# Kernel tuning notes

Measured on AMD Instinct MI355X. Metric: run time of the kernel, lower is better.

## Reference

```python
import jax, jax.numpy as jnp
import numpy as np

D_MODEL = 1024
NUM_HEADS = 16
HEAD_DIM = D_MODEL // NUM_HEADS

def setup_inputs() -> dict:
    key = jax.random.key(0)
    ks = jax.random.split(key, 5)
    B, T = 4, 2048
    x = jax.random.normal(ks[0], (B, T, D_MODEL), dtype=jnp.float32)
    s = 1.0 / np.sqrt(D_MODEL)
    W_qkv = jax.random.normal(ks[1], (D_MODEL, 3 * D_MODEL), dtype=jnp.float32) * s
    b_qkv = jnp.zeros((3 * D_MODEL,), dtype=jnp.float32)
    W_out = jax.random.normal(ks[2], (D_MODEL, D_MODEL), dtype=jnp.float32) * s
    b_out = jnp.zeros((D_MODEL,), dtype=jnp.float32)
    return {"x": x, "W_qkv": W_qkv, "b_qkv": b_qkv, "W_out": W_out, "b_out": b_out}

def reference(x, W_qkv, b_qkv, W_out, b_out):
    B, T, C = x.shape
    H, Dh = NUM_HEADS, HEAD_DIM
    qkv = x @ W_qkv + b_qkv                      # [B,T,3C]
    qkv = qkv.reshape(B, T, 3, H, Dh)
    q = jnp.transpose(qkv[:, :, 0], (0, 2, 1, 3))  # [B,H,T,Dh]
    k = jnp.transpose(qkv[:, :, 1], (0, 2, 1, 3))
    v = jnp.transpose(qkv[:, :, 2], (0, 2, 1, 3))
    scores = jnp.einsum('bhqd,bhkd->bhqk', q, k) / jnp.sqrt(jnp.asarray(Dh, x.dtype))
    weights = jax.nn.softmax(scores, axis=-1)
    out = jnp.einsum('bhqk,bhkd->bhqd', weights, v)  # [B,H,T,Dh]
    out = jnp.transpose(out, (0, 2, 1, 3)).reshape(B, T, C)
    return out @ W_out + b_out
```

## Files before the change

### kernel.cpp

```cpp
#include <hip/hip_runtime.h>
#include <stdint.h>

typedef __bf16 bf16x8 __attribute__((ext_vector_type(8)));
typedef float f32x4 __attribute__((ext_vector_type(4)));
typedef float f32x16 __attribute__((ext_vector_type(16)));

static constexpr int BB = 4, TT = 2048, CC = 1024, HH = 16, DH = 64;
static constexpr int MM = BB * TT;
static constexpr int N1 = 3 * CC;
static constexpr int KK = CC;

__device__ __forceinline__ unsigned short f2bf(float f) {
  uint32_t u = __builtin_bit_cast(uint32_t, f);
  u += 0x7FFFu + ((u >> 16) & 1u);
  return (unsigned short)(u >> 16);
}

__device__ __forceinline__ void async16(const void* g, void* l) {
  __builtin_amdgcn_global_load_lds((const __attribute__((address_space(1))) void*)g,
                                   (__attribute__((address_space(3))) void*)l, 16, 0, 0);
}

__global__ __launch_bounds__(256) void k_cvt(const float* __restrict__ src,
                                             unsigned short* __restrict__ dst) {
  int i = blockIdx.x * 256 + threadIdx.x;
  const float4* s = (const float4*)src + (size_t)i * 2;
  float4 a = s[0], b = s[1];
  union { unsigned short h[8]; uint4 v; } o;
  o.h[0] = f2bf(a.x); o.h[1] = f2bf(a.y); o.h[2] = f2bf(a.z); o.h[3] = f2bf(a.w);
  o.h[4] = f2bf(b.x); o.h[5] = f2bf(b.y); o.h[6] = f2bf(b.z); o.h[7] = f2bf(b.w);
  ((uint4*)dst)[i] = o.v;
}

__global__ __launch_bounds__(256) void k_tcvt(const float* __restrict__ src,
                                              unsigned short* __restrict__ dst,
                                              int R, int C) {
  __shared__ float tile[32][33];
  int tx = threadIdx.x & 31, ty = threadIdx.x >> 5;
  int c0 = blockIdx.x * 32, r0 = blockIdx.y * 32;
#pragma unroll
  for (int i = 0; i < 4; ++i)
    tile[ty + i * 8][tx] = src[(size_t)(r0 + ty + i * 8) * C + c0 + tx];
  __syncthreads();
#pragma unroll
  for (int i = 0; i < 4; ++i)
    dst[(size_t)(c0 + ty + i * 8) * R + r0 + tx] = f2bf(tile[tx][ty + i * 8]);
}


#define LDA(Ab, mf, ksl) \
  (*(const bf16x8*)&(Ab)[wm * 8192 + ((mf) * 16 + l15) * 64 + \
                         ((((ksl) * 4 + l16) ^ (l15 & 7)) * 8)])
#define LDB(Bb, nf, ksl) \
  (*(const bf16x8*)&(Bb)[(wn >> 1) * 8192 + ((wn & 1) * 64 + (nf) * 16 + l15) * 64 + \
                         ((((ksl) * 4 + l16) ^ (l15 & 7)) * 8)])

struct AF4 { bf16x8 a00, a01, a10, a11; };

template <int Q, bool LOADB>
__device__ __forceinline__ AF4 phase_pre(const unsigned short* Ab, const unsigned short* Bb,
                                         int wm, int wn, int l15, int l16, bf16x8* bfr) {
  AF4 f;
  f.a00 = LDA(Ab, Q * 2, 0);     f.a01 = LDA(Ab, Q * 2, 1);
  f.a10 = LDA(Ab, Q * 2 + 1, 0); f.a11 = LDA(Ab, Q * 2 + 1, 1);
  if (LOADB) {
#pragma unroll
    for (int nf = 0; nf < 4; ++nf) {
      bfr[nf] = LDB(Bb, nf, 0);
      bfr[4 + nf] = LDB(Bb, nf, 1);
    }
  }
  return f;
}

template <int Q>
__device__ __forceinline__ void phase_mfma(const AF4& f, const bf16x8* bfr, f32x4 acc[8][4]) {
#pragma unroll
  for (int nf = 0; nf < 4; ++nf)
    acc[Q * 2][nf] = __builtin_amdgcn_mfma_f32_16x16x32_bf16(f.a00, bfr[nf], acc[Q * 2][nf], 0, 0, 0);
#pragma unroll
  for (int nf = 0; nf < 4; ++nf)
    acc[Q * 2][nf] = __builtin_amdgcn_mfma_f32_16x16x32_bf16(f.a01, bfr[4 + nf], acc[Q * 2][nf], 0, 0, 0);
#pragma unroll
  for (int nf = 0; nf < 4; ++nf)
    acc[Q * 2 + 1][nf] = __builtin_amdgcn_mfma_f32_16x16x32_bf16(f.a10, bfr[nf], acc[Q * 2 + 1][nf], 0, 0, 0);
#pragma unroll
  for (int nf = 0; nf < 4; ++nf)
    acc[Q * 2 + 1][nf] = __builtin_amdgcn_mfma_f32_16x16x32_bf16(f.a11, bfr[4 + nf], acc[Q * 2 + 1][nf], 0, 0, 0);
}

#define PHASE(Q, AB, BB_, LOADB, STAGES, WAITS)                       \
  { AF4 f_ = phase_pre<Q, LOADB>(AB, BB_, wm, wn, l15, l16, bfr);     \
    STAGES;                                                           \
    WAITS;                                                            \
    __builtin_amdgcn_s_barrier();                                     \
    asm volatile("s_waitcnt lgkmcnt(0)" ::: "memory");                \
    __builtin_amdgcn_sched_barrier(0);                                \
    __builtin_amdgcn_s_setprio(1);                                    \
    phase_mfma<Q>(f_, bfr, acc);                                      \
    __builtin_amdgcn_s_setprio(0);                                    \
    __builtin_amdgcn_s_barrier(); }

template <int MODE, int NBX>
__global__ __launch_bounds__(512, 2) void k_gemm8(
    const unsigned short* __restrict__ A, const unsigned short* __restrict__ Bt,
    const float* __restrict__ bias, int M, int N, int K,
    unsigned short* __restrict__ qo, unsigned short* __restrict__ ko,
    unsigned short* __restrict__ vo, float* __restrict__ fo) {
  __shared__ __attribute__((aligned(16))) unsigned short lds[65536];
  unsigned short* As0 = lds;
  unsigned short* As1 = lds + 16384;
  unsigned short* Bs0 = lds + 32768;
  unsigned short* Bs1 = lds + 49152;

  const int tid = threadIdx.x;
  const int lane = tid & 63;
  const int w = tid >> 6, wm = w >> 2, wn = w & 3;
  const int l15 = lane & 15, l16 = lane >> 4;

  const int nwg = gridDim.x;
  const int q8 = nwg >> 3;
  const int swz = ((int)blockIdx.x & 7) * q8 + ((int)blockIdx.x >> 3);
  const int m0 = (swz / NBX) * 256, n0 = (swz % NBX) * 256;

  f32x4 acc[8][4] = {};

  const int srow = tid >> 3;
  const int sg = ((tid & 7) ^ (srow & 7)) * 8;
  const int dOff = srow * 64 + (tid & 7) * 8;
  const unsigned short* aBase = A + (size_t)(m0 + srow) * K + sg;
  const unsigned short* bBase = Bt + (size_t)(n0 + srow) * K + sg;

#define STAGE_A(dst, kt, h)                                                          \
  { async16(aBase + (size_t)((h) * 128) * K + (kt) * 64, (dst) + (h) * 8192 + dOff); \
    async16(aBase + (size_t)((h) * 128 + 64) * K + (kt) * 64,                        \
            (dst) + (h) * 8192 + 4096 + dOff); }
#define STAGE_B(dst, kt, h)                                                          \
  { async16(bBase + (size_t)((h) * 128) * K + (kt) * 64, (dst) + (h) * 8192 + dOff); \
    async16(bBase + (size_t)((h) * 128 + 64) * K + (kt) * 64,                        \
            (dst) + (h) * 8192 + 4096 + dOff); }

  STAGE_A(As0, 0, 0); STAGE_A(As0, 0, 1);
  STAGE_B(Bs0, 0, 0); STAGE_B(Bs0, 0, 1);
  STAGE_B(Bs1, 1, 0); STAGE_B(Bs1, 1, 1);
  asm volatile("s_waitcnt vmcnt(0)" ::: "memory");
  __builtin_amdgcn_s_barrier();

  const int NITER = K / 128;
#pragma unroll 1
  for (int i = 0; i < NITER; ++i) {
    const bool more = (i + 1 < NITER);
    const int t1 = 2 * i + 1, t2k = 2 * i + 2, t3 = 2 * i + 3;
    bf16x8 bfr[8];
    PHASE(0, As0, Bs0, true,  { STAGE_A(As1, t1, 0); }, ((void)0));
    PHASE(1, As0, Bs0, false, { STAGE_A(As1, t1, 1); }, ((void)0));
    PHASE(2, As0, Bs0, false, { if (more) STAGE_B(Bs0, t2k, 0); }, ((void)0));
    PHASE(3, As0, Bs0, false, { if (more) STAGE_B(Bs0, t2k, 1); },
          { if (more) { asm volatile("s_waitcnt vmcnt(4)" ::: "memory"); }
            else      { asm volatile("s_waitcnt vmcnt(0)" ::: "memory"); } });
    PHASE(0, As1, Bs1, true,  { if (more) STAGE_A(As0, t2k, 0); }, ((void)0));
    PHASE(1, As1, Bs1, false, { if (more) STAGE_A(As0, t2k, 1); }, ((void)0));
    PHASE(2, As1, Bs1, false, { if (more) STAGE_B(Bs1, t3, 0); }, ((void)0));
    PHASE(3, As1, Bs1, false, { if (more) STAGE_B(Bs1, t3, 1); },
          { asm volatile("s_waitcnt vmcnt(4)" ::: "memory"); });
  }

  if (MODE == 0) {
    const int sel = n0 >> 10;
    if (sel < 2) {
      const float qs = (sel == 0) ? 0.180336892f : 1.0f;
      float bj[4];
#pragma unroll
      for (int nf = 0; nf < 4; ++nf) bj[nf] = bias[n0 + wn * 64 + nf * 16 + l15];
#pragma unroll
      for (int mf = 0; mf < 8; ++mf)
#pragma unroll
        for (int nf = 0; nf < 4; ++nf)
#pragma unroll
          for (int r = 0; r < 4; ++r) {
            const int row = wm * 128 + mf * 16 + l16 * 4 + r;
            const int col = wn * 64 + nf * 16 + l15;
            lds[row * 256 + (((col >> 3) ^ (row & 31)) * 8) + (col & 7)] =
                f2bf((acc[mf][nf][r] + bj[nf]) * qs);
          }
      __syncthreads();
      const int row = tid >> 1, half = tid & 1;
      const int gm = m0 + row, bb2 = gm >> 11, t2 = gm & 2047;
      const int hb = ((n0 & 1023) >> 6) + half * 2;
      unsigned short* base = (sel == 0 ? qo : ko);
#pragma unroll
      for (int hh = 0; hh < 2; ++hh) {
        unsigned short* dst = base + ((size_t)(bb2 * HH + hb + hh) * TT + t2) * DH;
#pragma unroll
        for (int g = 0; g < 8; ++g) {
          const int cg = half * 16 + hh * 8 + g;
          bf16x8 v = *(const bf16x8*)&lds[row * 256 + ((cg ^ (row & 31)) * 8)];
          *(bf16x8*)&dst[g * 8] = v;
        }
      }
    } else {
#pragma unroll
      for (int mf = 0; mf < 8; ++mf)
#pragma unroll
        for (int nf = 0; nf < 4; ++nf) {
          const int gn = n0 + wn * 64 + nf * 16 + l15;
          const float bj = bias[gn];
          const int h = (gn & 1023) >> 6, d = gn & 63;
          const int gm0 = m0 + wm * 128 + mf * 16 + l16 * 4;
          const int bb2 = gm0 >> 11, t0 = gm0 & 2047;
          union { unsigned short s[4]; uint2 u; } pk;
#pragma unroll
          for (int r = 0; r < 4; ++r) pk.s[r] = f2bf(acc[mf][nf][r] + bj);
          *(uint2*)&vo[((size_t)(bb2 * HH + h) * DH + d) * TT + t0] = pk.u;
        }
    }
  } else {
#pragma unroll
    for (int mf = 0; mf < 8; ++mf)
#pragma unroll
      for (int nf = 0; nf < 4; ++nf) {
        const int gn = n0 + wn * 64 + nf * 16 + l15;
        const float bj = bias[gn];
#pragma unroll
        for (int r = 0; r < 4; ++r) {
          const int gm = m0 + wm * 128 + mf * 16 + l16 * 4 + r;
          fo[(size_t)gm * N + gn] = acc[mf][nf][r] + bj;
        }
      }
  }
#undef STAGE_A
#undef STAGE_B
}

__global__ __launch_bounds__(256, 2) void k_attn(
    const unsigned short* __restrict__ Q,
    const unsigned short* __restrict__ Kx,
    const unsigned short* __restrict__ Vt,
    unsigned short* __restrict__ At,
    float neg16) {
  __shared__ __attribute__((aligned(16))) unsigned short Ks[2][64 * 64];
  __shared__ __attribute__((aligned(16))) unsigned short Vs[2][64 * 64];
  const int tid = threadIdx.x, lane = tid & 63, w = tid >> 6;
  const int l31 = lane & 31, hi5 = lane >> 5;
  const int id = blockIdx.x;
  const int bh = (id & 7) + ((id >> 7) << 3);
  const int qb = (id >> 3) & 15;
  const int q0 = qb * 128 + w * 32;
  const unsigned short* Qp = Q + (size_t)bh * TT * DH;
  const unsigned short* Kp = Kx + (size_t)bh * TT * DH;
  const unsigned short* Vp = Vt + (size_t)bh * DH * TT;

  bf16x8 qf[4];
#pragma unroll
  for (int j = 0; j < 4; ++j)
    qf[j] = *(const bf16x8*)&Qp[(size_t)(q0 + l31) * DH + j * 16 + hi5 * 8];

  f32x16 cinit;
#pragma unroll
  for (int r = 0; r < 16; ++r) cinit[r] = neg16;

  const int srow = tid >> 3;
  const int sg = ((tid & 7) ^ (srow & 7)) * 8;

  float l8[8];
#pragma unroll
  for (int r = 0; r < 8; ++r) l8[r] = 0.f;
  f32x16 oacc[2] = {};

#pragma unroll
  for (int i = 0; i < 2; ++i) {
    async16(Kp + (size_t)(i * 32 + srow) * DH + sg, &Ks[0][i * 2048 + tid * 8]);
    async16(Vp + (size_t)(i * 32 + srow) * TT + sg, &Vs[0][i * 2048 + tid * 8]);
  }
  __syncthreads();

#pragma unroll 2
  for (int kt = 0; kt < TT / 64; ++kt) {
    const int cur = kt & 1;
    if (kt + 1 < TT / 64) {
      const int kv1 = (kt + 1) * 64;
#pragma unroll
      for (int i = 0; i < 2; ++i) {
        async16(Kp + (size_t)(kv1 + i * 32 + srow) * DH + sg,
                &Ks[cur ^ 1][i * 2048 + tid * 8]);
        async16(Vp + (size_t)(i * 32 + srow) * TT + kv1 + sg,
                &Vs[cur ^ 1][i * 2048 + tid * 8]);
      }
    }

    f32x16 sacc[2];
    __builtin_amdgcn_s_setprio(1);
#pragma unroll
    for (int t = 0; t < 2; ++t) {
      bf16x8 kf = *(const bf16x8*)&Ks[cur][(t * 32 + l31) * 64 +
                      ((hi5 ^ (l31 & 7)) * 8)];
      sacc[t] = __builtin_amdgcn_mfma_f32_32x32x16_bf16(kf, qf[0], cinit, 0, 0, 0);
    }
#pragma unroll
    for (int ks16 = 1; ks16 < 4; ++ks16) {
#pragma unroll
      for (int t = 0; t < 2; ++t) {
        bf16x8 kf = *(const bf16x8*)&Ks[cur][(t * 32 + l31) * 64 +
                        (((ks16 * 2 + hi5) ^ (l31 & 7)) * 8)];
        sacc[t] = __builtin_amdgcn_mfma_f32_32x32x16_bf16(kf, qf[ks16], sacc[t], 0, 0, 0);
      }
    }
    __builtin_amdgcn_s_setprio(0);
    asm volatile("" : "+v"(sacc[0]), "+v"(sacc[1]));

#pragma unroll
    for (int t = 0; t < 2; ++t)
#pragma unroll
      for (int r = 0; r < 16; ++r)
        sacc[t][r] = __builtin_amdgcn_exp2f(sacc[t][r]);
#pragma unroll
    for (int r = 0; r < 8; ++r)
      l8[r] += (sacc[0][r] + sacc[0][r + 8]) + (sacc[1][r] + sacc[1][r + 8]);

    uint32_t wpk[16];
#pragma unroll
    for (int t = 0; t < 2; ++t) {
      union { __bf16 h[16]; uint32_t u[8]; } pk;
#pragma unroll
      for (int r = 0; r < 16; ++r) pk.h[r] = (__bf16)sacc[t][r];
#pragma unroll
      for (int j = 0; j < 8; ++j) wpk[t * 8 + j] = pk.u[j];
    }
    uint32_t xw[8];
#pragma unroll
    for (int t = 0; t < 2; ++t) {
      xw[t * 4 + 0] = __shfl_xor(hi5 ? wpk[t * 8 + 0] : wpk[t * 8 + 2], 32);
      xw[t * 4 + 1] = __shfl_xor(hi5 ? wpk[t * 8 + 1] : wpk[t * 8 + 3], 32);
      xw[t * 4 + 2] = __shfl_xor(hi5 ? wpk[t * 8 + 4] : wpk[t * 8 + 6], 32);
      xw[t * 4 + 3] = __shfl_xor(hi5 ? wpk[t * 8 + 5] : wpk[t * 8 + 7], 32);
    }

    __builtin_amdgcn_s_setprio(1);
#pragma unroll
    for (int ks = 0; ks < 4; ++ks) {
      const int t = ks >> 1, b = (ks & 1) * 4, o = t * 8, xb = t * 4 + (ks & 1) * 2;
      union { uint32_t u[4]; bf16x8 v; } pu;
      pu.u[0] = hi5 ? xw[xb] : wpk[o + b];
      pu.u[1] = hi5 ? xw[xb + 1] : wpk[o + b + 1];
      pu.u[2] = hi5 ? wpk[o + b + 2] : xw[xb];
      pu.u[3] = hi5 ? wpk[o + b + 3] : xw[xb + 1];
#pragma unroll
      for (int dt = 0; dt < 2; ++dt) {
        bf16x8 vf = *(const bf16x8*)&Vs[cur][(dt * 32 + l31) * 64 +
                        (((ks * 2 + hi5) ^ (l31 & 7)) * 8)];
        oacc[dt] = __builtin_amdgcn_mfma_f32_32x32x16_bf16(vf, pu.v, oacc[dt], 0, 0, 0);
      }
    }
    __builtin_amdgcn_s_setprio(0);
    __syncthreads();
  }

  float l = ((l8[0] + l8[4]) + (l8[1] + l8[5])) +
            ((l8[2] + l8[6]) + (l8[3] + l8[7]));
  l += __shfl_xor(l, 32);

  const float il = 1.0f / l;
  unsigned short* bw = &Ks[0][0] + w * 2048;
#pragma unroll
  for (int dt = 0; dt < 2; ++dt)
#pragma unroll
    for (int j = 0; j < 8; ++j) {
      const int dl = (j & 1) * 2 + (j >> 1) * 8 + hi5 * 4;
      const int d = dt * 32 + dl;
      const uint32_t pk = (uint32_t)f2bf(oacc[dt][2 * j] * il) |
                          ((uint32_t)f2bf(oacc[dt][2 * j + 1] * il) << 16);
      const int g = d >> 3, gi = (d >> 1) & 3;
      *(uint32_t*)&bw[l31 * 64 + ((g ^ (l31 & 7)) * 8) + gi * 2] = pk;
    }
  __syncthreads();
  const int bb = bh >> 4, hd = bh & 15;
#pragma unroll
  for (int i = 0; i < 4; ++i) {
    const int row = i * 8 + (lane >> 3);
    const int g = lane & 7;
    bf16x8 vv = *(const bf16x8*)&bw[row * 64 + ((g ^ (row & 7)) * 8)];
    *(bf16x8*)&At[((size_t)bb * TT + q0 + row) * CC + hd * DH + g * 8] = vv;
  }
}

extern "C" void kernel_launch(void* const* d_in, const int* in_sizes, int n_in,
                              void* d_out, int out_size, void* d_ws, size_t ws_size,
                              hipStream_t stream) {
  const float* x = (const float*)d_in[0];
  const float* Wqkv = (const float*)d_in[1];
  const float* bqkv = (const float*)d_in[2];
  const float* Wout = (const float*)d_in[3];
  const float* bout = (const float*)d_in[4];
  float* out = (float*)d_out;

  char* ws = (char*)d_ws;
  unsigned short* Xb  = (unsigned short*)(ws);
  unsigned short* WqT = (unsigned short*)(ws + (16ull << 20));
  unsigned short* WoT = (unsigned short*)(ws + (22ull << 20));
  unsigned short* Qb  = (unsigned short*)(ws + (24ull << 20));
  unsigned short* Kb  = (unsigned short*)(ws + (40ull << 20));
  unsigned short* Vt  = (unsigned short*)(ws + (56ull << 20));
  unsigned short* At  = (unsigned short*)(ws + (72ull << 20));

  k_cvt<<<dim3((MM * KK) / (256 * 8)), 256, 0, stream>>>(x, Xb);
  k_tcvt<<<dim3(N1 / 32, KK / 32), 256, 0, stream>>>(Wqkv, WqT, KK, N1);
  k_tcvt<<<dim3(CC / 32, KK / 32), 256, 0, stream>>>(Wout, WoT, KK, CC);
  k_gemm8<0, 12><<<dim3((N1 / 256) * (MM / 256)), 512, 0, stream>>>(
      Xb, WqT, bqkv, MM, N1, KK, Qb, Kb, Vt, nullptr);
  k_attn<<<dim3(BB * HH * (TT / 128)), 256, 0, stream>>>(Qb, Kb, Vt, At, -16.0f);
  k_gemm8<1, 4><<<dim3((CC / 256) * (MM / 256)), 512, 0, stream>>>(
      At, WoT, bout, MM, CC, KK, nullptr, nullptr, nullptr, out);
}
```

Baseline: 212.7 us.

## Use smaller-tile GEMM for output projection and relax attention loop barriers

The output projection moves from the 256x256-tile pipelined GEMM to a new 128x128-tile kernel with 256 threads. That launches 512 workgroups instead of 128, so more compute units are filled. The new kernel has no double buffering and no LDS swizzle, so load latency and LDS bank conflicts may be exposed. The attention loop now always prefetches the next K/V tile and replaces `__syncthreads` with explicit `vmcnt`/`lgkmcnt` waits plus `s_barrier`, so loads overlap compute. The trade-off is that the last iteration reads one tile beyond the current head's K/V data.

```diff
diff --git a/kernel.cpp b/kernel.cpp
--- a/kernel.cpp
+++ b/kernel.cpp
@@ -46,7 +46,6 @@
   for (int i = 0; i < 4; ++i)
     dst[(size_t)(c0 + ty + i * 8) * R + r0 + tx] = f2bf(tile[tx][ty + i * 8]);
 }
-
 
 #define LDA(Ab, mf, ksl) \
   (*(const bf16x8*)&(Ab)[wm * 8192 + ((mf) * 16 + l15) * 64 + \
@@ -101,12 +100,12 @@
     __builtin_amdgcn_s_setprio(0);                                    \
     __builtin_amdgcn_s_barrier(); }
 
-template <int MODE, int NBX>
+template <int NBX>
 __global__ __launch_bounds__(512, 2) void k_gemm8(
     const unsigned short* __restrict__ A, const unsigned short* __restrict__ Bt,
     const float* __restrict__ bias, int M, int N, int K,
     unsigned short* __restrict__ qo, unsigned short* __restrict__ ko,
-    unsigned short* __restrict__ vo, float* __restrict__ fo) {
+    unsigned short* __restrict__ vo) {
   __shared__ __attribute__((aligned(16))) unsigned short lds[65536];
   unsigned short* As0 = lds;
   unsigned short* As1 = lds + 16384;
@@ -165,54 +164,37 @@
           { asm volatile("s_waitcnt vmcnt(4)" ::: "memory"); });
   }
 
-  if (MODE == 0) {
-    const int sel = n0 >> 10;
-    if (sel < 2) {
-      const float qs = (sel == 0) ? 0.180336892f : 1.0f;
-      float bj[4];
-#pragma unroll
-      for (int nf = 0; nf < 4; ++nf) bj[nf] = bias[n0 + wn * 64 + nf * 16 + l15];
-#pragma unroll
-      for (int mf = 0; mf < 8; ++mf)
-#pragma unroll
-        for (int nf = 0; nf < 4; ++nf)
-#pragma unroll
-          for (int r = 0; r < 4; ++r) {
-            const int row = wm * 128 + mf * 16 + l16 * 4 + r;
-            const int col = wn * 64 + nf * 16 + l15;
-            lds[row * 256 + (((col >> 3) ^ (row & 31)) * 8) + (col & 7)] =
-                f2bf((acc[mf][nf][r] + bj[nf]) * qs);
-          }
-      __syncthreads();
-      const int row = tid >> 1, half = tid & 1;
-      const int gm = m0 + row, bb2 = gm >> 11, t2 = gm & 2047;
-      const int hb = ((n0 & 1023) >> 6) + half * 2;
-      unsigned short* base = (sel == 0 ? qo : ko);
-#pragma unroll
-      for (int hh = 0; hh < 2; ++hh) {
-        unsigned short* dst = base + ((size_t)(bb2 * HH + hb + hh) * TT + t2) * DH;
-#pragma unroll
-        for (int g = 0; g < 8; ++g) {
-          const int cg = half * 16 + hh * 8 + g;
-          bf16x8 v = *(const bf16x8*)&lds[row * 256 + ((cg ^ (row & 31)) * 8)];
-          *(bf16x8*)&dst[g * 8] = v;
+  const int sel = n0 >> 10;
+  if (sel < 2) {
+    const float qs = (sel == 0) ? 0.180336892f : 1.0f;
+    float bj[4];
+#pragma unroll
+    for (int nf = 0; nf < 4; ++nf) bj[nf] = bias[n0 + wn * 64 + nf * 16 + l15];
+#pragma unroll
+    for (int mf = 0; mf < 8; ++mf)
+#pragma unroll
+      for (int nf = 0; nf < 4; ++nf)
+#pragma unroll
+        for (int r = 0; r < 4; ++r) {
+          const int row = wm * 128 + mf * 16 + l16 * 4 + r;
+          const int col = wn * 64 + nf * 16 + l15;
+          lds[row * 256 + (((col >> 3) ^ (row & 31)) * 8) + (col & 7)] =
+              f2bf((acc[mf][nf][r] + bj[nf]) * qs);
         }
+    __syncthreads();
+    const int row = tid >> 1, half = tid & 1;
+    const int gm = m0 + row, bb2 = gm >> 11, t2 = gm & 2047;
+    const int hb = ((n0 & 1023) >> 6) + half * 2;
+    unsigned short* base = (sel == 0 ? qo : ko);
+#pragma unroll
+    for (int hh = 0; hh < 2; ++hh) {
+      unsigned short* dst = base + ((size_t)(bb2 * HH + hb + hh) * TT + t2) * DH;
+#pragma unroll
+      for (int g = 0; g < 8; ++g) {
+        const int cg = half * 16 + hh * 8 + g;
+        bf16x8 v = *(const bf16x8*)&lds[row * 256 + ((cg ^ (row & 31)) * 8)];
+        *(bf16x8*)&dst[g * 8] = v;
       }
-    } else {
-#pragma unroll
-      for (int mf = 0; mf < 8; ++mf)
-#pragma unroll
-        for (int nf = 0; nf < 4; ++nf) {
-          const int gn = n0 + wn * 64 + nf * 16 + l15;
-          const float bj = bias[gn];
-          const int h = (gn & 1023) >> 6, d = gn & 63;
-          const int gm0 = m0 + wm * 128 + mf * 16 + l16 * 4;
-          const int bb2 = gm0 >> 11, t0 = gm0 & 2047;
-          union { unsigned short s[4]; uint2 u; } pk;
-#pragma unroll
-          for (int r = 0; r < 4; ++r) pk.s[r] = f2bf(acc[mf][nf][r] + bj);
-          *(uint2*)&vo[((size_t)(bb2 * HH + h) * DH + d) * TT + t0] = pk.u;
-        }
     }
   } else {
 #pragma unroll
@@ -221,15 +203,76 @@
       for (int nf = 0; nf < 4; ++nf) {
         const int gn = n0 + wn * 64 + nf * 16 + l15;
         const float bj = bias[gn];
-#pragma unroll
-        for (int r = 0; r < 4; ++r) {
-          const int gm = m0 + wm * 128 + mf * 16 + l16 * 4 + r;
-          fo[(size_t)gm * N + gn] = acc[mf][nf][r] + bj;
-        }
+        const int h = (gn & 1023) >> 6, d = gn & 63;
+        const int gm0 = m0 + wm * 128 + mf * 16 + l16 * 4;
+        const int bb2 = gm0 >> 11, t0 = gm0 & 2047;
+        union { unsigned short s[4]; uint2 u; } pk;
+#pragma unroll
+        for (int r = 0; r < 4; ++r) pk.s[r] = f2bf(acc[mf][nf][r] + bj);
+        *(uint2*)&vo[((size_t)(bb2 * HH + h) * DH + d) * TT + t0] = pk.u;
       }
   }
 #undef STAGE_A
 #undef STAGE_B
+}
+
+__global__ __launch_bounds__(256) void k_gemmB(
+    const unsigned short* __restrict__ A, const unsigned short* __restrict__ Bt,
+    const float* __restrict__ bias, int M, int N, int K,
+    float* __restrict__ fo) {
+  __shared__ __attribute__((aligned(16))) unsigned short As[128 * 64];
+  __shared__ __attribute__((aligned(16))) unsigned short Bs[128 * 64];
+  const int tid = threadIdx.x;
+  const int lane = tid & 63;
+  const int w = tid >> 6, wr = w >> 1, wc = w & 1;
+  const int l15 = lane & 15, l16 = lane >> 4;
+  const int m0 = blockIdx.y * 128, n0 = blockIdx.x * 128;
+
+  f32x4 acc[4][4] = {};
+
+  const unsigned short* aSrc = A + (size_t)(m0 + (tid >> 3)) * K + (tid & 7) * 8;
+  const unsigned short* bSrc = Bt + (size_t)(n0 + (tid >> 3)) * K + (tid & 7) * 8;
+  unsigned short* aDst = &As[tid * 8];
+  unsigned short* bDst = &Bs[tid * 8];
+
+#pragma unroll 1
+  for (int k0 = 0; k0 < K; k0 += 64) {
+#pragma unroll
+    for (int i = 0; i < 4; ++i) {
+      async16(aSrc + (size_t)i * 32 * K + k0, aDst + i * 2048);
+      async16(bSrc + (size_t)i * 32 * K + k0, bDst + i * 2048);
+    }
+    __syncthreads();
+#pragma unroll
+    for (int ks = 0; ks < 2; ++ks) {
+      bf16x8 af[4], bfr[4];
+#pragma unroll
+      for (int i = 0; i < 4; ++i)
+        af[i] = *(const bf16x8*)&As[(wr * 64 + i * 16 + l15) * 64 + ks * 32 + l16 * 8];
+#pragma unroll
+      for (int j = 0; j < 4; ++j)
+        bfr[j] = *(const bf16x8*)&Bs[(wc * 64 + j * 16 + l15) * 64 + ks * 32 + l16 * 8];
+#pragma unroll
+      for (int i = 0; i < 4; ++i)
+#pragma unroll
+        for (int j = 0; j < 4; ++j)
+          acc[i][j] = __builtin_amdgcn_mfma_f32_16x16x32_bf16(af[i], bfr[j], acc[i][j], 0, 0, 0);
+    }
+    __syncthreads();
+  }
+
+#pragma unroll
+  for (int i = 0; i < 4; ++i)
+#pragma unroll
+    for (int j = 0; j < 4; ++j) {
+      const int gn = n0 + wc * 64 + j * 16 + l15;
+      const float bj = bias[gn];
+#pragma unroll
+      for (int r = 0; r < 4; ++r) {
+        const int gm = m0 + wr * 64 + i * 16 + l16 * 4 + r;
+        fo[(size_t)gm * N + gn] = acc[i][j][r] + bj;
+      }
+    }
 }
 
 __global__ __launch_bounds__(256, 2) void k_attn(
@@ -272,21 +315,21 @@
     async16(Kp + (size_t)(i * 32 + srow) * DH + sg, &Ks[0][i * 2048 + tid * 8]);
     async16(Vp + (size_t)(i * 32 + srow) * TT + sg, &Vs[0][i * 2048 + tid * 8]);
   }
-  __syncthreads();
 
 #pragma unroll 2
   for (int kt = 0; kt < TT / 64; ++kt) {
     const int cur = kt & 1;
-    if (kt + 1 < TT / 64) {
-      const int kv1 = (kt + 1) * 64;
-#pragma unroll
-      for (int i = 0; i < 2; ++i) {
-        async16(Kp + (size_t)(kv1 + i * 32 + srow) * DH + sg,
-                &Ks[cur ^ 1][i * 2048 + tid * 8]);
-        async16(Vp + (size_t)(i * 32 + srow) * TT + kv1 + sg,
-                &Vs[cur ^ 1][i * 2048 + tid * 8]);
-      }
-    }
+    const int kv1 = (kt + 1) * 64;
+#pragma unroll
+    for (int i = 0; i < 2; ++i) {
+      async16(Kp + (size_t)(kv1 + i * 32 + srow) * DH + sg,
+              &Ks[cur ^ 1][i * 2048 + tid * 8]);
+      async16(Vp + (size_t)(i * 32 + srow) * TT + kv1 + sg,
+              &Vs[cur ^ 1][i * 2048 + tid * 8]);
+    }
+    asm volatile("s_waitcnt vmcnt(4)" ::: "memory");
+    __builtin_amdgcn_sched_barrier(0);
+    __builtin_amdgcn_s_barrier();
 
     f32x16 sacc[2];
     __builtin_amdgcn_s_setprio(1);
@@ -352,8 +395,13 @@
       }
     }
     __builtin_amdgcn_s_setprio(0);
-    __syncthreads();
-  }
+    asm volatile("s_waitcnt lgkmcnt(0)" ::: "memory");
+    __builtin_amdgcn_sched_barrier(0);
+    __builtin_amdgcn_s_barrier();
+  }
+
+  asm volatile("s_waitcnt vmcnt(0)" ::: "memory");
+  __builtin_amdgcn_s_barrier();
 
   float l = ((l8[0] + l8[4]) + (l8[1] + l8[5])) +
             ((l8[2] + l8[6]) + (l8[3] + l8[7]));
@@ -405,9 +453,9 @@
   k_cvt<<<dim3((MM * KK) / (256 * 8)), 256, 0, stream>>>(x, Xb);
   k_tcvt<<<dim3(N1 / 32, KK / 32), 256, 0, stream>>>(Wqkv, WqT, KK, N1);
   k_tcvt<<<dim3(CC / 32, KK / 32), 256, 0, stream>>>(Wout, WoT, KK, CC);
-  k_gemm8<0, 12><<<dim3((N1 / 256) * (MM / 256)), 512, 0, stream>>>(
-      Xb, WqT, bqkv, MM, N1, KK, Qb, Kb, Vt, nullptr);
+  k_gemm8<12><<<dim3((N1 / 256) * (MM / 256)), 512, 0, stream>>>(
+      Xb, WqT, bqkv, MM, N1, KK, Qb, Kb, Vt);
   k_attn<<<dim3(BB * HH * (TT / 128)), 256, 0, stream>>>(Qb, Kb, Vt, At, -16.0f);
-  k_gemm8<1, 4><<<dim3((CC / 256) * (MM / 256)), 512, 0, stream>>>(
-      At, WoT, bout, MM, CC, KK, nullptr, nullptr, nullptr, out);
-}
+  k_gemmB<<<dim3(CC / 128, MM / 128), 256, 0, stream>>>(
+      At, WoT, bout, MM, CC, KK, out);
+}
```

After: 216.9 us. Within noise of the previous version (+2.0%).

## Shrink GEMM tiles to 256x128 with reworked phase schedule and epilogue

Applied to the files above, without the earlier changes.

Both projection GEMMs move from 256x256 to 256x128 output tiles. Per-wave accumulators are halved, B staging now covers 128 rows, and each k-step runs two phases instead of four, with new waitcnt values and a new LDS epilogue layout. The aim is to double the workgroup count (768 and 256 tiles) for better CU fill on the MI355X and to cut LDS and register use. The cost is lower arithmetic intensity per tile, more A-tile reloads, and fewer MFMAs per barrier to hide the sync overhead.

```diff
diff --git a/kernel.cpp b/kernel.cpp
--- a/kernel.cpp
+++ b/kernel.cpp
@@ -48,82 +48,81 @@
 }
 
 
-#define LDA(Ab, mf, ksl) \
-  (*(const bf16x8*)&(Ab)[wm * 8192 + ((mf) * 16 + l15) * 64 + \
+#define LDA4(Ab, mf, ksl) \
+  (*(const bf16x8*)&(Ab)[(wm * 128 + (mf) * 16 + l15) * 64 + \
                          ((((ksl) * 4 + l16) ^ (l15 & 7)) * 8)])
-#define LDB(Bb, nf, ksl) \
-  (*(const bf16x8*)&(Bb)[(wn >> 1) * 8192 + ((wn & 1) * 64 + (nf) * 16 + l15) * 64 + \
+#define LDB4(Bb, nf, ksl) \
+  (*(const bf16x8*)&(Bb)[(wn * 32 + (nf) * 16 + l15) * 64 + \
                          ((((ksl) * 4 + l16) ^ (l15 & 7)) * 8)])
 
-struct AF4 { bf16x8 a00, a01, a10, a11; };
-
-template <int Q, bool LOADB>
-__device__ __forceinline__ AF4 phase_pre(const unsigned short* Ab, const unsigned short* Bb,
-                                         int wm, int wn, int l15, int l16, bf16x8* bfr) {
-  AF4 f;
-  f.a00 = LDA(Ab, Q * 2, 0);     f.a01 = LDA(Ab, Q * 2, 1);
-  f.a10 = LDA(Ab, Q * 2 + 1, 0); f.a11 = LDA(Ab, Q * 2 + 1, 1);
+struct AF8 { bf16x8 a[8]; };
+
+template <int P, bool LOADB>
+__device__ __forceinline__ AF8 phase_pre4(const unsigned short* Ab, const unsigned short* Bb,
+                                          int wm, int wn, int l15, int l16, bf16x8* bfr) {
+  AF8 f;
+#pragma unroll
+  for (int mf = 0; mf < 4; ++mf) {
+    f.a[mf * 2] = LDA4(Ab, P * 4 + mf, 0);
+    f.a[mf * 2 + 1] = LDA4(Ab, P * 4 + mf, 1);
+  }
   if (LOADB) {
 #pragma unroll
-    for (int nf = 0; nf < 4; ++nf) {
-      bfr[nf] = LDB(Bb, nf, 0);
-      bfr[4 + nf] = LDB(Bb, nf, 1);
+    for (int nf = 0; nf < 2; ++nf) {
+      bfr[nf * 2] = LDB4(Bb, nf, 0);
+      bfr[nf * 2 + 1] = LDB4(Bb, nf, 1);
     }
   }
   return f;
 }
 
-template <int Q>
-__device__ __forceinline__ void phase_mfma(const AF4& f, const bf16x8* bfr, f32x4 acc[8][4]) {
-#pragma unroll
-  for (int nf = 0; nf < 4; ++nf)
-    acc[Q * 2][nf] = __builtin_amdgcn_mfma_f32_16x16x32_bf16(f.a00, bfr[nf], acc[Q * 2][nf], 0, 0, 0);
-#pragma unroll
-  for (int nf = 0; nf < 4; ++nf)
-    acc[Q * 2][nf] = __builtin_amdgcn_mfma_f32_16x16x32_bf16(f.a01, bfr[4 + nf], acc[Q * 2][nf], 0, 0, 0);
-#pragma unroll
-  for (int nf = 0; nf < 4; ++nf)
-    acc[Q * 2 + 1][nf] = __builtin_amdgcn_mfma_f32_16x16x32_bf16(f.a10, bfr[nf], acc[Q * 2 + 1][nf], 0, 0, 0);
-#pragma unroll
-  for (int nf = 0; nf < 4; ++nf)
-    acc[Q * 2 + 1][nf] = __builtin_amdgcn_mfma_f32_16x16x32_bf16(f.a11, bfr[4 + nf], acc[Q * 2 + 1][nf], 0, 0, 0);
-}
-
-#define PHASE(Q, AB, BB_, LOADB, STAGES, WAITS)                       \
-  { AF4 f_ = phase_pre<Q, LOADB>(AB, BB_, wm, wn, l15, l16, bfr);     \
+template <int P>
+__device__ __forceinline__ void phase_mfma4(const AF8& f, const bf16x8* bfr, f32x4 acc[8][2]) {
+#pragma unroll
+  for (int mf = 0; mf < 4; ++mf)
+#pragma unroll
+    for (int nf = 0; nf < 2; ++nf) {
+      acc[P * 4 + mf][nf] = __builtin_amdgcn_mfma_f32_16x16x32_bf16(
+          f.a[mf * 2], bfr[nf * 2], acc[P * 4 + mf][nf], 0, 0, 0);
+      acc[P * 4 + mf][nf] = __builtin_amdgcn_mfma_f32_16x16x32_bf16(
+          f.a[mf * 2 + 1], bfr[nf * 2 + 1], acc[P * 4 + mf][nf], 0, 0, 0);
+    }
+}
+
+#define PHASE4(P, AB, BB_, LOADB, STAGES, WAITS)                      \
+  { AF8 f_ = phase_pre4<P, LOADB>(AB, BB_, wm, wn, l15, l16, bfr);    \
     STAGES;                                                           \
     WAITS;                                                            \
     __builtin_amdgcn_s_barrier();                                     \
     asm volatile("s_waitcnt lgkmcnt(0)" ::: "memory");                \
     __builtin_amdgcn_sched_barrier(0);                                \
     __builtin_amdgcn_s_setprio(1);                                    \
-    phase_mfma<Q>(f_, bfr, acc);                                      \
+    phase_mfma4<P>(f_, bfr, acc);                                     \
     __builtin_amdgcn_s_setprio(0);                                    \
     __builtin_amdgcn_s_barrier(); }
 
 template <int MODE, int NBX>
-__global__ __launch_bounds__(512, 2) void k_gemm8(
+__global__ __launch_bounds__(512, 2) void k_gemm4(
     const unsigned short* __restrict__ A, const unsigned short* __restrict__ Bt,
     const float* __restrict__ bias, int M, int N, int K,
     unsigned short* __restrict__ qo, unsigned short* __restrict__ ko,
     unsigned short* __restrict__ vo, float* __restrict__ fo) {
-  __shared__ __attribute__((aligned(16))) unsigned short lds[65536];
+  __shared__ __attribute__((aligned(16))) unsigned short lds[49152];
   unsigned short* As0 = lds;
   unsigned short* As1 = lds + 16384;
   unsigned short* Bs0 = lds + 32768;
-  unsigned short* Bs1 = lds + 49152;
+  unsigned short* Bs1 = lds + 40960;
 
   const int tid = threadIdx.x;
   const int lane = tid & 63;
   const int w = tid >> 6, wm = w >> 2, wn = w & 3;
   const int l15 = lane & 15, l16 = lane >> 4;
 
-  const int nwg = gridDim.x;
-  const int q8 = nwg >> 3;
+  const int q8 = (int)gridDim.x >> 3;
   const int swz = ((int)blockIdx.x & 7) * q8 + ((int)blockIdx.x >> 3);
-  const int m0 = (swz / NBX) * 256, n0 = (swz % NBX) * 256;
-
-  f32x4 acc[8][4] = {};
+  const int m0 = (swz / NBX) * 256, n0 = (swz % NBX) * 128;
+
+  f32x4 acc[8][2] = {};
 
   const int srow = tid >> 3;
   const int sg = ((tid & 7) ^ (srow & 7)) * 8;
@@ -135,14 +134,13 @@
   { async16(aBase + (size_t)((h) * 128) * K + (kt) * 64, (dst) + (h) * 8192 + dOff); \
     async16(aBase + (size_t)((h) * 128 + 64) * K + (kt) * 64,                        \
             (dst) + (h) * 8192 + 4096 + dOff); }
-#define STAGE_B(dst, kt, h)                                                          \
-  { async16(bBase + (size_t)((h) * 128) * K + (kt) * 64, (dst) + (h) * 8192 + dOff); \
-    async16(bBase + (size_t)((h) * 128 + 64) * K + (kt) * 64,                        \
-            (dst) + (h) * 8192 + 4096 + dOff); }
+#define STAGE_B(dst, kt)                                                             \
+  { async16(bBase + (kt) * 64, (dst) + dOff);                                        \
+    async16(bBase + (size_t)64 * K + (kt) * 64, (dst) + 4096 + dOff); }
 
   STAGE_A(As0, 0, 0); STAGE_A(As0, 0, 1);
-  STAGE_B(Bs0, 0, 0); STAGE_B(Bs0, 0, 1);
-  STAGE_B(Bs1, 1, 0); STAGE_B(Bs1, 1, 1);
+  STAGE_B(Bs0, 0);
+  STAGE_B(Bs1, 1);
   asm volatile("s_waitcnt vmcnt(0)" ::: "memory");
   __builtin_amdgcn_s_barrier();
 
@@ -150,60 +148,57 @@
 #pragma unroll 1
   for (int i = 0; i < NITER; ++i) {
     const bool more = (i + 1 < NITER);
-    const int t1 = 2 * i + 1, t2k = 2 * i + 2, t3 = 2 * i + 3;
-    bf16x8 bfr[8];
-    PHASE(0, As0, Bs0, true,  { STAGE_A(As1, t1, 0); }, ((void)0));
-    PHASE(1, As0, Bs0, false, { STAGE_A(As1, t1, 1); }, ((void)0));
-    PHASE(2, As0, Bs0, false, { if (more) STAGE_B(Bs0, t2k, 0); }, ((void)0));
-    PHASE(3, As0, Bs0, false, { if (more) STAGE_B(Bs0, t2k, 1); },
-          { if (more) { asm volatile("s_waitcnt vmcnt(4)" ::: "memory"); }
-            else      { asm volatile("s_waitcnt vmcnt(0)" ::: "memory"); } });
-    PHASE(0, As1, Bs1, true,  { if (more) STAGE_A(As0, t2k, 0); }, ((void)0));
-    PHASE(1, As1, Bs1, false, { if (more) STAGE_A(As0, t2k, 1); }, ((void)0));
-    PHASE(2, As1, Bs1, false, { if (more) STAGE_B(Bs1, t3, 0); }, ((void)0));
-    PHASE(3, As1, Bs1, false, { if (more) STAGE_B(Bs1, t3, 1); },
-          { asm volatile("s_waitcnt vmcnt(4)" ::: "memory"); });
+    const int tb = 2 * i + 1, t2k = 2 * i + 2, t3 = 2 * i + 3;
+    bf16x8 bfr[4];
+    PHASE4(0, As0, Bs0, true,
+           { STAGE_A(As1, tb, 0); STAGE_A(As1, tb, 1); }, ((void)0));
+    PHASE4(1, As0, Bs0, false,
+           { if (more) STAGE_B(Bs0, t2k); },
+           { if (more) { asm volatile("s_waitcnt vmcnt(2)" ::: "memory"); }
+             else      { asm volatile("s_waitcnt vmcnt(0)" ::: "memory"); } });
+    PHASE4(0, As1, Bs1, true,
+           { if (more) { STAGE_A(As0, t2k, 0); STAGE_A(As0, t2k, 1); } }, ((void)0));
+    PHASE4(1, As1, Bs1, false,
+           { if (more) STAGE_B(Bs1, t3); },
+           { if (more) { asm volatile("s_waitcnt vmcnt(2)" ::: "memory"); } });
   }
 
   if (MODE == 0) {
     const int sel = n0 >> 10;
     if (sel < 2) {
       const float qs = (sel == 0) ? 0.180336892f : 1.0f;
-      float bj[4];
-#pragma unroll
-      for (int nf = 0; nf < 4; ++nf) bj[nf] = bias[n0 + wn * 64 + nf * 16 + l15];
+      float bj[2];
+#pragma unroll
+      for (int nf = 0; nf < 2; ++nf) bj[nf] = bias[n0 + wn * 32 + nf * 16 + l15];
 #pragma unroll
       for (int mf = 0; mf < 8; ++mf)
 #pragma unroll
-        for (int nf = 0; nf < 4; ++nf)
+        for (int nf = 0; nf < 2; ++nf)
 #pragma unroll
           for (int r = 0; r < 4; ++r) {
             const int row = wm * 128 + mf * 16 + l16 * 4 + r;
-            const int col = wn * 64 + nf * 16 + l15;
-            lds[row * 256 + (((col >> 3) ^ (row & 31)) * 8) + (col & 7)] =
+            const int col = wn * 32 + nf * 16 + l15;
+            lds[row * 128 + (col >> 6) * 64 +
+                ((((col >> 3) & 7) ^ (row & 7)) * 8) + (col & 7)] =
                 f2bf((acc[mf][nf][r] + bj[nf]) * qs);
           }
       __syncthreads();
       const int row = tid >> 1, half = tid & 1;
       const int gm = m0 + row, bb2 = gm >> 11, t2 = gm & 2047;
-      const int hb = ((n0 & 1023) >> 6) + half * 2;
-      unsigned short* base = (sel == 0 ? qo : ko);
-#pragma unroll
-      for (int hh = 0; hh < 2; ++hh) {
-        unsigned short* dst = base + ((size_t)(bb2 * HH + hb + hh) * TT + t2) * DH;
-#pragma unroll
-        for (int g = 0; g < 8; ++g) {
-          const int cg = half * 16 + hh * 8 + g;
-          bf16x8 v = *(const bf16x8*)&lds[row * 256 + ((cg ^ (row & 31)) * 8)];
-          *(bf16x8*)&dst[g * 8] = v;
-        }
+      const int h2 = ((n0 & 1023) >> 6) + half;
+      unsigned short* dst = (sel == 0 ? qo : ko) +
+          ((size_t)(bb2 * HH + h2) * TT + t2) * DH;
+#pragma unroll
+      for (int g = 0; g < 8; ++g) {
+        bf16x8 v = *(const bf16x8*)&lds[row * 128 + half * 64 + ((g ^ (row & 7)) * 8)];
+        *(bf16x8*)&dst[g * 8] = v;
       }
     } else {
 #pragma unroll
       for (int mf = 0; mf < 8; ++mf)
 #pragma unroll
-        for (int nf = 0; nf < 4; ++nf) {
-          const int gn = n0 + wn * 64 + nf * 16 + l15;
+        for (int nf = 0; nf < 2; ++nf) {
+          const int gn = n0 + wn * 32 + nf * 16 + l15;
           const float bj = bias[gn];
           const int h = (gn & 1023) >> 6, d = gn & 63;
           const int gm0 = m0 + wm * 128 + mf * 16 + l16 * 4;
@@ -218,8 +213,8 @@
 #pragma unroll
     for (int mf = 0; mf < 8; ++mf)
 #pragma unroll
-      for (int nf = 0; nf < 4; ++nf) {
-        const int gn = n0 + wn * 64 + nf * 16 + l15;
+      for (int nf = 0; nf < 2; ++nf) {
+        const int gn = n0 + wn * 32 + nf * 16 + l15;
         const float bj = bias[gn];
 #pragma unroll
         for (int r = 0; r < 4; ++r) {
@@ -405,9 +400,9 @@
   k_cvt<<<dim3((MM * KK) / (256 * 8)), 256, 0, stream>>>(x, Xb);
   k_tcvt<<<dim3(N1 / 32, KK / 32), 256, 0, stream>>>(Wqkv, WqT, KK, N1);
   k_tcvt<<<dim3(CC / 32, KK / 32), 256, 0, stream>>>(Wout, WoT, KK, CC);
-  k_gemm8<0, 12><<<dim3((N1 / 256) * (MM / 256)), 512, 0, stream>>>(
+  k_gemm4<0, 24><<<dim3((MM / 256) * (N1 / 128)), 512, 0, stream>>>(
       Xb, WqT, bqkv, MM, N1, KK, Qb, Kb, Vt, nullptr);
   k_attn<<<dim3(BB * HH * (TT / 128)), 256, 0, stream>>>(Qb, Kb, Vt, At, -16.0f);
-  k_gemm8<1, 4><<<dim3((CC / 256) * (MM / 256)), 512, 0, stream>>>(
+  k_gemm4<1, 8><<<dim3((MM / 256) * (CC / 128)), 512, 0, stream>>>(
       At, WoT, bout, MM, CC, KK, nullptr, nullptr, nullptr, out);
 }
```

Result: faster. 200.0 us (-6.0%).
